# Optimization experiments

Measured on AMD Instinct MI355X. Metric: run time of the kernel, lower is better.

## Reference

```python
import jax, jax.numpy as jnp
import numpy as np

ISIZE = 512; NHEAD = 8; NNOD = 8; MAXP = 5; NEDGE = 34; TAU = 1.0; EPS = 1e-6
B = 4; SLEN = 1024

def _ln(x, g, b):
    m = x.mean(-1, keepdims=True)
    v = ((x - m) ** 2).mean(-1, keepdims=True)
    return (x - m) * jax.lax.rsqrt(v + EPS) * g + b

def _qmask(nsrc):
    # q_mask_full: edge 0 (encoder source) is masked out for the q path
    m = np.zeros((nsrc, 5), bool); m[0, :] = True
    return m.reshape(-1)

def _routing(node_p, edge_p):
    # Host-side argmax routing; mirrors the .item() syncs in the torch forward.
    node_p = np.asarray(node_p); edge_p = np.asarray(edge_p)
    routes, lind = [], 0
    for c in range(NNOD):
        nsrc = min(c + 2, MAXP); snode = c - nsrc
        ep = edge_p[:, lind:lind + nsrc, :].reshape(3, -1)
        qm = _qmask(nsrc)
        nact = int(np.argmax(node_p[c]))
        qsel = int(np.argmax(np.where(qm, -np.inf, ep[0])))
        r = dict(lind=lind, nsrc=nsrc, snode=snode, act=nact, q=qsel, k=None, v=None, ktype=None, km=None, vmode=None)
        if nact < 7:
            km = qm if nact > 0 else None
            kl = ep[1] if km is None else np.where(km, -np.inf, ep[1])
            r['k'] = int(np.argmax(kl)); r['km'] = km
            r['ktype'] = -2 if r['k'] // 5 == 0 else -1
            if nact < 5:
                if nact == 0 and r['ktype'] == -2:
                    r['v'] = int(np.argmax(ep[2][:5])); r['vmode'] = 'first5'
                else:
                    vl = ep[2] if km is None else np.where(km, -np.inf, ep[2])
                    r['v'] = int(np.argmax(vl)); r['vmode'] = 'full'
        routes.append(r); lind += nsrc
    return routes

def _selw(logits, mask, sel):
    # GumbleNormDrop (eval): softmax over masked logits, weight of selected entry
    if mask is not None:
        logits = jnp.where(jnp.asarray(mask), -jnp.inf, logits)
    return jax.nn.softmax(logits / TAU)[sel]

def _edge_op(x, e, op, eW, eb, eg, ebe):
    # ops 0/1/2: LN->Linear with relu/gelu/identity (cost isize^2+3*isize); 3: Linear; 4: identity
    if op == 4:
        return x
    if op == 3:
        return x @ eW[e] + eb[e]
    h = _ln(x, eg[e], ebe[e]) @ eW[e] + eb[e]
    return jax.nn.relu(h) if op == 0 else (jax.nn.gelu(h) if op == 1 else h)

def _mha(q, k, v, Wn, bn, gn, bln, mask):
    Bq, Sq, D = q.shape; dh = D // NHEAD; Sk = k.shape[1]
    qn = _ln(q, gn, bln)
    qh = (qn @ Wn[0] + bn[0]).reshape(Bq, Sq, NHEAD, dh).transpose(0, 2, 1, 3)
    kh = (k @ Wn[1] + bn[1]).reshape(Bq, Sk, NHEAD, dh).transpose(0, 2, 1, 3)
    vh = (v @ Wn[2] + bn[2]).reshape(Bq, v.shape[1], NHEAD, dh).transpose(0, 2, 1, 3)
    s = jnp.einsum('bhqd,bhkd->bhqk', qh, kh) / np.float32(np.sqrt(dh))
    if mask is not None:
        s = jnp.where(mask[:, :, None, :], -1e9, s)  # [B,1,Sk] -> [B,1,1,Sk]
    o = jnp.einsum('bhqk,bhkd->bhqd', jax.nn.softmax(s, -1), vh)
    o = o.transpose(0, 2, 1, 3).reshape(Bq, Sq, D)
    return q + o @ Wn[3] + bn[3]

def _node_op(q, k, v, act, Wn, bn, gn, bln, mask):
    if act == 0: return _mha(q, k, v, Wn, bn, gn, bln, mask)
    if act == 1: return q + (jax.nn.gelu(q @ Wn[0] + bn[0]) * (k @ Wn[1] + bn[1])) @ Wn[3] + bn[3]
    if act == 2: return _ln(q + k + v, gn, bln)
    if act == 3: return q + jax.nn.relu(q @ Wn[0] + k @ Wn[1] + v @ Wn[2]) @ Wn[3] + bn[3]
    if act == 4: return q * jax.nn.sigmoid(k) + v
    if act == 5: return q + jax.nn.gelu(k @ Wn[1] + bn[1])
    if act == 6: return q + k
    return _ln(q, gn, bln)  # act 7: unary

def _forward(inpute, inputo, node_p, edge_p, eW, eb, eg, ebe, nW, nb, ng, nbe, og, obe, src_pad_mask, tgt_pad_mask, routes):
    outs = {-2: inpute, -1: inputo}
    processed = set()
    for c, r in enumerate(routes):
        lind, snode = r['lind'], r['snode']
        epq, epk, epv = (edge_p[i, lind:lind + r['nsrc'], :].reshape(-1) for i in range(3))
        qm = _qmask(r['nsrc'])
        aw = jax.nn.softmax(node_p[c] / TAU)[r['act']]
        def take(sel, logits, mask):
            se, op = sel // 5, sel % 5
            inn = -2 if se == 0 else snode + se
            processed.add(inn)
            return _selw(logits, mask, sel) * _edge_op(outs[inn], lind + se, op, eW, eb, eg, ebe)
        qv = take(r['q'], epq, qm)
        kv = take(r['k'], epk, r['km']) if r['k'] is not None else None
        if r['v'] is None:
            vv = None
        elif r['vmode'] == 'first5':
            vv = take(r['v'], epv[:5], None)
        else:
            vv = take(r['v'], epv, r['km'])
        mask = None if r['act'] == 7 else (tgt_pad_mask if r['ktype'] == -1 else src_pad_mask)
        outs[c] = aw * _node_op(qv, kv, vv, r['act'], nW[c], nb[c], ng[c], nbe[c], mask)
    rem = [outs[i] for i in range(NNOD) if i not in processed]
    o = rem[0]
    for t in rem[1:]:
        o = o + t
    return _ln(o, og, obe)

def setup_inputs():
    key = jax.random.key(0)
    ks = jax.random.split(key, 8)
    s = 0.02
    return {
        'inpute': jax.random.normal(ks[0], (B, SLEN, ISIZE), jnp.float32),
        'inputo': jax.random.normal(ks[1], (B, SLEN, ISIZE), jnp.float32),
        'node_p': jax.random.normal(ks[2], (NNOD, 8), jnp.float32),
        'edge_p': jax.random.normal(ks[3], (3, NEDGE, 5), jnp.float32),
        'edge_W': jax.random.normal(ks[4], (NEDGE, ISIZE, ISIZE), jnp.float32) * s,
        'edge_b': jnp.zeros((NEDGE, ISIZE), jnp.float32),
        'edge_g': jnp.ones((NEDGE, ISIZE), jnp.float32),
        'edge_beta': jnp.zeros((NEDGE, ISIZE), jnp.float32),
        'node_W': jax.random.normal(ks[5], (NNOD, 4, ISIZE, ISIZE), jnp.float32) * s,
        'node_b': jnp.zeros((NNOD, 4, ISIZE), jnp.float32),
        'node_g': jnp.ones((NNOD, ISIZE), jnp.float32),
        'node_beta': jnp.zeros((NNOD, ISIZE), jnp.float32),
        'out_g': jnp.ones((ISIZE,), jnp.float32),
        'out_beta': jnp.zeros((ISIZE,), jnp.float32),
        'src_pad_mask': jnp.zeros((B, 1, SLEN), bool),
        'tgt_pad_mask': jnp.zeros((B, 1, SLEN), bool),
    }

def reference(inpute, inputo, node_p, edge_p, edge_W, edge_b, edge_g, edge_beta, node_W, node_b, node_g, node_beta, out_g, out_beta, src_pad_mask, tgt_pad_mask):
    routes = _routing(node_p, edge_p)
    return _forward(inpute, inputo, node_p, edge_p, edge_W, edge_b, edge_g, edge_beta, node_W, node_b, node_g, node_beta, out_g, out_beta, src_pad_mask, tgt_pad_mask, routes)
```

## Files before the change

### kernel.cpp

```cpp
#include <hip/hip_runtime.h>
#include <hip/hip_bf16.h>
#include <math.h>

#define NTOK 4096
#define DIM  512
#define NNODC 8
#define NEDGEC 34
#define NMAT  98
#define NBUF 4

typedef unsigned short u16;
typedef unsigned int   u32;

typedef __attribute__((ext_vector_type(8))) short bf16x8;
typedef __attribute__((ext_vector_type(4))) float f32x4;

__device__ __forceinline__ float b2f(u16 u){ return __uint_as_float(((u32)u) << 16); }
__device__ __forceinline__ u16 f2b(float f){
    u32 x = __float_as_uint(f);
    u32 r = x + 0x7FFFu + ((x >> 16) & 1u);
    return (u16)(r >> 16);
}
__device__ __forceinline__ float ldp(const void* p, int i, int isbf){
    return isbf ? b2f(((const u16*)p)[i]) : ((const float*)p)[i];
// ... 227 lines not shown
    const size_t base = ((size_t)blockIdx.x*256 + threadIdx.x) * 8;
    if (R->isbf){
        *(uint4*)(Xb0 + base) = *(const uint4*)((const u16*)ie + base);
        *(uint4*)(Xb1 + base) = *(const uint4*)((const u16*)io + base);
    } else {
        const float* a = (const float*)ie + base;
        const float* b = (const float*)io + base;
        u16 oa[8], ob[8];
        #pragma unroll
        for (int j = 0; j < 8; j++){ oa[j] = f2b(a[j]); ob[j] = f2b(b[j]); }
        *(uint4*)(Xb0 + base) = *(const uint4*)oa;
        *(uint4*)(Xb1 + base) = *(const uint4*)ob;
    }
}

struct __align__(16) LGS { u16 A[NBUF][64*64]; u16 B[NBUF][64*64]; };
struct __align__(16) LGU {
    union { LGS g; float st[64*68]; } u;
    float2 rowst[64];
};

__device__ void lean_gemm(LGU& smu, int isbf, int nsrc, int m0, int n0,
        const u16* __restrict__ A0, const u16* __restrict__ A1, const u16* __restrict__ A2,
        const u16* __restrict__ W0, const u16* __restrict__ W1, const u16* __restrict__ W2,
        const void* bias, int actMode,
        const float* __restrict__ uv,
        const u16* __restrict__ residB, float scale,
        u16* __restrict__ outB)
{
    LGS& sm = smu.u.g;
    const int tid = threadIdx.x;
    const int w = tid >> 6, lane = tid & 63;
    const int wr = w >> 1, wc = w & 1;
    const int l15 = lane & 15, quad = lane >> 4;
    const int NT = nsrc * 8;

    const int rsw = lane >> 3;
    const int c16 = lane & 7;
    const int rA  = w*16 + rsw;
    const int kx  = (c16 ^ rsw) << 3;

    auto stage = [&](int buf, int it){
        const int s = it >> 3, kt = it & 7;
        const u16* Ab = (s == 0) ? A0 : ((s == 1) ? A1 : A2);
        const u16* Wb = (s == 0) ? W0 : ((s == 1) ? W1 : W2);
        const size_t ka = (size_t)kt*64 + kx;
        const u16* ga = Ab + (size_t)(m0 + rA)*DIM + ka;
        const u16* gb = Wb + (size_t)(n0 + rA)*DIM + ka;
        u16* la = &sm.A[buf][rA*64 + c16*8];
        u16* lb = &sm.B[buf][rA*64 + c16*8];
        gload16(ga,          la);
        gload16(ga + 8*DIM,  la + 8*64);
        gload16(gb,          lb);
        gload16(gb + 8*DIM,  lb + 8*64);
    };

    f32x4 acc[2][2];
    #pragma unroll
    for (int i = 0; i < 2; i++)
        #pragma unroll
        for (int j = 0; j < 2; j++) acc[i][j] = (f32x4){0.f,0.f,0.f,0.f};

    float ssum = 0.f, ssq = 0.f;

    stage(0, 0);
    if (NT > 1) stage(1, 1);

    for (int it = 0; it < NT; it++){
        const int buf = it & (NBUF-1);
        if (it + 2 < NT) stage((it + 2) & (NBUF-1), it + 2);
        const int newer = (NT - 1 - it) < 2 ? (NT - 1 - it) : 2;
        if (newer == 2)      asm volatile("s_waitcnt vmcnt(8)" ::: "memory");
        else if (newer == 1) asm volatile("s_waitcnt vmcnt(4)" ::: "memory");
        else                 asm volatile("s_waitcnt vmcnt(0)" ::: "memory");
        __builtin_amdgcn_s_barrier();
        __builtin_amdgcn_sched_barrier(0);
        #pragma unroll
        for (int kc = 0; kc < 2; kc++){
            const int sl = (((kc*4 + quad) ^ (l15 & 7)) << 3);
            bf16x8 af0 = *(const bf16x8*)&sm.A[buf][(wr*32      + l15)*64 + sl];
            bf16x8 af1 = *(const bf16x8*)&sm.A[buf][(wr*32 + 16 + l15)*64 + sl];
            bf16x8 bf0 = *(const bf16x8*)&sm.B[buf][(wc*32      + l15)*64 + sl];
            bf16x8 bf1 = *(const bf16x8*)&sm.B[buf][(wc*32 + 16 + l15)*64 + sl];
            acc[0][0] = __builtin_amdgcn_mfma_f32_16x16x32_bf16(af0, bf0, acc[0][0], 0, 0, 0);
            acc[0][1] = __builtin_amdgcn_mfma_f32_16x16x32_bf16(af0, bf1, acc[0][1], 0, 0, 0);
            acc[1][0] = __builtin_amdgcn_mfma_f32_16x16x32_bf16(af1, bf0, acc[1][0], 0, 0, 0);
            acc[1][1] = __builtin_amdgcn_mfma_f32_16x16x32_bf16(af1, bf1, acc[1][1], 0, 0, 0);
        }
        if (uv){
            const int srow = w*16 + l15;
            #pragma unroll
            for (int ch = 0; ch < 2; ch++){
                const int gc = quad*2 + ch;
                const bf16x8 xv = *(const bf16x8*)&sm.A[buf][srow*64 + ((gc ^ (srow&7))<<3)];
                #pragma unroll
                for (int t2 = 0; t2 < 8; t2++){
                    const float fx = b2f((u16)xv[t2]);
                    ssum += fx; ssq += fx*fx;
                }
            }
        }
    }

    if (uv){
        ssum += __shfl_xor(ssum, 16); ssq += __shfl_xor(ssq, 16);
        ssum += __shfl_xor(ssum, 32); ssq += __shfl_xor(ssq, 32);
        if (quad == 0){
            const float mu = ssum*(1.0f/512.0f);
            const float rstd = rsqrtf(ssq*(1.0f/512.0f) - mu*mu + 1e-6f);
            smu.rowst[w*16 + l15] = make_float2(mu, rstd);
        }
    }
    __syncthreads();

    float* st = smu.u.st;
    #pragma unroll
    for (int i = 0; i < 2; i++){
        const int rowl = wr*32 + i*16 + quad*4;
        float al[4], bet[4];
        if (uv){
            #pragma unroll
            for (int rg = 0; rg < 4; rg++){
                const float2 ms = smu.rowst[rowl + rg];
                al[rg] = ms.y; bet[rg] = -ms.y*ms.x;
            }
        }
        #pragma unroll
        for (int j = 0; j < 2; j++){
            const int coll = wc*32 + j*16 + l15;
            const float bv = bias ? ldp(bias, n0 + coll, isbf) : 0.f;
            const float un = uv ? uv[n0 + coll]       : 0.f;
            const float vn = uv ? uv[512 + n0 + coll] : 0.f;
            #pragma unroll
            for (int rg = 0; rg < 4; rg++){
                float v = acc[i][j][rg];
                if (uv) v = al[rg]*v + bet[rg]*un + vn;
                v += bv;
                if (actMode == 1) v = fmaxf(v, 0.f);
                else if (actMode == 2) v = gelu_t(v);
                st[(rowl + rg)*68 + coll] = v;
            }
        }
    }
    __syncthreads();
    #pragma unroll
    for (int t = 0; t < 2; t++){
        const int cid = tid + 256*t;
        const int rowl = cid >> 3, cg = (cid & 7)*8;
        float v[8];
        *(float4*)&v[0] = *(const float4*)&st[rowl*68 + cg];
        *(float4*)&v[4] = *(const float4*)&st[rowl*68 + cg + 4];
        const size_t go = (size_t)(m0 + rowl)*DIM + n0 + cg;
        if (residB){
            uint4 ru = *(const uint4*)(residB + go);
            const u16* rp = (const u16*)&ru;
            #pragma unroll
            for (int j2 = 0; j2 < 8; j2++) v[j2] += b2f(rp[j2]);
        }
        u16 o[8];
        #pragma unroll
        for (int j2 = 0; j2 < 8; j2++) o[j2] = f2b(v[j2]*scale);
        *(uint4*)(outB + go) = *(const uint4*)o;
    }
}

__device__ __forceinline__ void tile_remap(int* m0, int* n0){
    const int lin = blockIdx.y*64 + blockIdx.x;
    const int xcd = lin & 7, idx = lin >> 3;
    *m0 = (xcd*8 + (idx & 7)) * 64;
    *n0 = (idx >> 3) * 64;
}

__device__ __forceinline__ const void* subp(const void* p, size_t elemOff, int isbf){
    return isbf ? (const void*)((const u16*)p + elemOff) : (const void*)((const float*)p + elemOff);
}

__global__ __launch_bounds__(256, 2) void edge_gemm(const Routes* __restrict__ R, int c,
        const u16* __restrict__ Xb,
        u16* QVb, u16* KVb, u16* VVb,
        const u16* __restrict__ Wt, const float* __restrict__ UV, const void* eb){
    __shared__ LGU sm;
    const int isbf = R->isbf;
    const int z = blockIdx.z;
    int has, slot, e, op; float w; u16* outB;
    if (z == 0){ has = 1;            slot = R->q_slot[c]; e = R->q_e[c]; op = R->q_op[c]; w = R->qw[c]; outB = QVb; }
    else if (z == 1){ has = R->k_has[c]; slot = R->k_slot[c]; e = R->k_e[c]; op = R->k_op[c]; w = R->kw[c]; outB = KVb; }
    else        { has = R->v_has[c]; slot = R->v_slot[c]; e = R->v_e[c]; op = R->v_op[c]; w = R->vw[c]; outB = VVb; }
    if (!has) return;
    if (op == 4){
        const int tid = threadIdx.x;
        const int r  = blockIdx.x*64 + (tid >> 2);
        const int c0 = blockIdx.y*64 + (tid & 3)*16;
        const u16* src = Xb + (size_t)slot*NTOK*DIM + (size_t)r*DIM + c0;
        const size_t off = (size_t)r*DIM + c0;
        #pragma unroll
        for (int t = 0; t < 2; t++){
            uint4 u = *(const uint4*)(src + t*8);
            const u16* up = (const u16*)&u;
            u16 o[8];
            #pragma unroll
            for (int j = 0; j < 8; j++) o[j] = f2b(w*b2f(up[j]));
            *(uint4*)(outB + off + t*8) = *(const uint4*)o;
        }
        return;
    }
    const u16* A = Xb + (size_t)slot*NTOK*DIM;
    int m0, n0; tile_remap(&m0, &n0);
    const size_t msz = (size_t)DIM*DIM;
    if (op < 3){
        const int f = c*3 + z;
        const int actMode = (op == 0) ? 1 : ((op == 1) ? 2 : 0);
        lean_gemm(sm, isbf, 1, m0, n0, A, nullptr, nullptr,
                  Wt + (size_t)(66 + f)*msz, nullptr, nullptr,
                  subp(eb, (size_t)e*DIM, isbf), actMode,
                  UV + (size_t)f*1024, nullptr, w, outB);
    } else {
        lean_gemm(sm, isbf, 1, m0, n0, A, nullptr, nullptr,
                  Wt + (size_t)e*msz, nullptr, nullptr,
                  subp(eb, (size_t)e*DIM, isbf), 0,
                  nullptr, nullptr, w, outB);
    }
}

__global__ __launch_bounds__(256) void mid1(const Routes* __restrict__ R, int c,
        const u16* __restrict__ QVb, const u16* __restrict__ KVb, const u16* __restrict__ VVb,
        u16* __restrict__ outcb,
        const void* ng, const void* nbeta){
    const int act = R->act[c];
    if (act == 0 || act == 1 || act == 3 || act == 5) return;
    const int isbf = R->isbf;
    const float aw = R->aw[c];
    const int tid = threadIdx.x, wid = tid >> 6, lane = tid & 63;
    const int row = blockIdx.x*4 + wid;
    const size_t roff = (size_t)row*DIM;
    float x[8];
    #pragma unroll
    for (int j = 0; j < 2; j++){
        ushort4 u = *(const ushort4*)(QVb + roff + lane*4 + j*256);
        x[j*4+0] = b2f(u.x); x[j*4+1] = b2f(u.y); x[j*4+2] = b2f(u.z); x[j*4+3] = b2f(u.w);
    }
    if (act == 4 || act == 6 || act == 2){
        float k[8], v[8];
        #pragma unroll
        for (int j = 0; j < 2; j++){
            ushort4 u = *(const ushort4*)(KVb + roff + lane*4 + j*256);
            k[j*4+0] = b2f(u.x); k[j*4+1] = b2f(u.y); k[j*4+2] = b2f(u.z); k[j*4+3] = b2f(u.w);
        }
        if (act != 6){
            #pragma unroll
            for (int j = 0; j < 2; j++){
                ushort4 u = *(const ushort4*)(VVb + roff + lane*4 + j*256);
                v[j*4+0] = b2f(u.x); v[j*4+1] = b2f(u.y); v[j*4+2] = b2f(u.z); v[j*4+3] = b2f(u.w);
            }
        }
        if (act == 4){
            #pragma unroll
            for (int j = 0; j < 2; j++){
                u16 o[4];
                #pragma unroll
                for (int t = 0; t < 4; t++) o[t] = f2b(aw*(x[j*4+t]*sigm(k[j*4+t]) + v[j*4+t]));
                *(ushort4*)(outcb + roff + lane*4 + j*256) = *(const ushort4*)o;
            }
            return;
        }
        if (act == 6){
            #pragma unroll
            for (int j = 0; j < 2; j++){
                u16 o[4];
                #pragma unroll
                for (int t = 0; t < 4; t++) o[t] = f2b(aw*(x[j*4+t] + k[j*4+t]));
                *(ushort4*)(outcb + roff + lane*4 + j*256) = *(const ushort4*)o;
            }
            return;
        }
        #pragma unroll
        for (int j = 0; j < 8; j++) x[j] += k[j] + v[j];
    }
    float s = 0.f, q2 = 0.f;
    #pragma unroll
    for (int j = 0; j < 8; j++){ s += x[j]; q2 += x[j]*x[j]; }
    #pragma unroll
    for (int m = 1; m < 64; m <<= 1){ s += __shfl_xor(s, m); q2 += __shfl_xor(q2, m); }
    const float mu = s*(1.0f/512.0f);
    const float rstd = rsqrtf(q2*(1.0f/512.0f) - mu*mu + 1e-6f);
    #pragma unroll
    for (int j = 0; j < 2; j++){
        const int col = lane*4 + j*256;
        u16 o[4];
        #pragma unroll
        for (int t = 0; t < 4; t++)
            o[t] = f2b(aw*((x[j*4+t] - mu)*rstd*ldp(ng, c*DIM + col + t, isbf) + ldp(nbeta, c*DIM + col + t, isbf)));
        *(ushort4*)(outcb + roff + col) = *(const ushort4*)o;
    }
}

__global__ __launch_bounds__(256, 2) void node_gemm_a(const Routes* __restrict__ R, int c,
        const u16* __restrict__ QVb, const u16* __restrict__ KVb, const u16* __restrict__ VVb,
        u16* T1b, u16* T2b, u16* T3b,
        const u16* __restrict__ Wt, const float* __restrict__ UV, const void* nb){
    __shared__ LGU sm;
    const int isbf = R->isbf;
    const int act = R->act[c];
    const int z = blockIdx.z;
    const size_t msz = (size_t)DIM*DIM;
    const u16* W0 = Wt + (NEDGEC + (size_t)c*4 + 0)*msz;
    const u16* W1 = Wt + (NEDGEC + (size_t)c*4 + 1)*msz;
    const u16* W2 = Wt + (NEDGEC + (size_t)c*4 + 2)*msz;
// ... 18 lines not shown
            lean_gemm(sm, isbf, 1, m0, n0, KVb,0,0, W1,0,0, b1, 2, nullptr, nullptr, 1.f, T2b);
    } else {
        if (act == 0)
            lean_gemm(sm, isbf, 1, m0, n0, VVb,0,0, W2,0,0, b2, 0, nullptr, nullptr, 1.f, T3b);
    }
}

struct __align__(16) FS {
    float Qs[64][68];
    float KPs[64][68];
    float Vs[64][68];
    float red[64*16];
    float mrun[64], lrun[64], alph[64];
};

__global__ __launch_bounds__(256) void mid2(const Routes* __restrict__ R, int c,
        const u16* __restrict__ Q, const u16* __restrict__ K,
        const u16* __restrict__ V, u16* __restrict__ T4b){
    const int act = R->act[c];
    if (act == 1){
        const int bid = blockIdx.y*32 + blockIdx.x;
        const size_t base = ((size_t)bid*256 + threadIdx.x)*16;
        #pragma unroll
        for (int h = 0; h < 2; h++){
            uint4 ua = *(const uint4*)(Q + base + h*8);
            uint4 ub = *(const uint4*)(K + base + h*8);
            const u16* pa = (const u16*)&ua;
            const u16* pb = (const u16*)&ub;
            u16 o[8];
            #pragma unroll
            for (int j = 0; j < 8; j++) o[j] = f2b(b2f(pa[j]) * b2f(pb[j]));
            *(uint4*)(T4b + base + h*8) = *(const uint4*)o;
        }
        return;
    }
    if (act != 0) return;
    __shared__ FS sm;
    const int tid = threadIdx.x;
    const int tx = tid & 15, ty = tid >> 4;
    const int b = blockIdx.x >> 3, h = blockIdx.x & 7;
    const int q0 = blockIdx.y * 64;
    const size_t baseQ = ((size_t)b*1024 + q0)*DIM + h*64;
    {
        const int r = tid >> 2, ch = tid & 3;
        const u16* qp = Q + baseQ + (size_t)r*DIM + ch*16;
        #pragma unroll
        for (int t = 0; t < 4; t++){
            ushort4 u = *(const ushort4*)(qp + t*4);
            sm.Qs[r][ch*16 + t*4 + 0] = b2f(u.x);
            sm.Qs[r][ch*16 + t*4 + 1] = b2f(u.y);
            sm.Qs[r][ch*16 + t*4 + 2] = b2f(u.z);
            sm.Qs[r][ch*16 + t*4 + 3] = b2f(u.w);
        }
    }
    if (tid < 64){ sm.mrun[tid] = -INFINITY; sm.lrun[tid] = 0.f; }
    float o[4][4];
    #pragma unroll
    for (int i = 0; i < 4; i++)
        #pragma unroll
        for (int j = 0; j < 4; j++) o[i][j] = 0.f;
    __syncthreads();

    for (int kt = 0; kt < 16; kt++){
        const size_t baseK = ((size_t)b*1024 + kt*64)*DIM + h*64;
        {
            const int r = tid >> 2, ch = tid & 3;
            const u16* kp = K + baseK + (size_t)r*DIM + ch*16;
            const u16* vp = V + baseK + (size_t)r*DIM + ch*16;
            #pragma unroll
            for (int t = 0; t < 4; t++){
                ushort4 uk = *(const ushort4*)(kp + t*4);
                ushort4 uv2 = *(const ushort4*)(vp + t*4);
                sm.KPs[r][ch*16 + t*4 + 0] = b2f(uk.x);
                sm.KPs[r][ch*16 + t*4 + 1] = b2f(uk.y);
                sm.KPs[r][ch*16 + t*4 + 2] = b2f(uk.z);
                sm.KPs[r][ch*16 + t*4 + 3] = b2f(uk.w);
                sm.Vs [r][ch*16 + t*4 + 0] = b2f(uv2.x);
                sm.Vs [r][ch*16 + t*4 + 1] = b2f(uv2.y);
                sm.Vs [r][ch*16 + t*4 + 2] = b2f(uv2.z);
                sm.Vs [r][ch*16 + t*4 + 3] = b2f(uv2.w);
            }
        }
        __syncthreads();
        float s[4][4];
        #pragma unroll
        for (int i = 0; i < 4; i++)
            #pragma unroll
            for (int j = 0; j < 4; j++) s[i][j] = 0.f;
        for (int d = 0; d < 64; d += 4){
            float4 qv[4], kv[4];
            #pragma unroll
            for (int i = 0; i < 4; i++) qv[i] = *(const float4*)&sm.Qs[ty*4+i][d];
            #pragma unroll
            for (int j = 0; j < 4; j++) kv[j] = *(const float4*)&sm.KPs[tx*4+j][d];
            #pragma unroll
            for (int i = 0; i < 4; i++)
                #pragma unroll
                for (int j = 0; j < 4; j++)
                    s[i][j] += qv[i].x*kv[j].x + qv[i].y*kv[j].y + qv[i].z*kv[j].z + qv[i].w*kv[j].w;
        }
        #pragma unroll
        for (int i = 0; i < 4; i++)
            #pragma unroll
            for (int j = 0; j < 4; j++) s[i][j] *= 0.125f;
        #pragma unroll
        for (int i = 0; i < 4; i++){
            float mx = fmaxf(fmaxf(s[i][0], s[i][1]), fmaxf(s[i][2], s[i][3]));
            sm.red[(ty*4+i)*16 + tx] = mx;
        }
        __syncthreads();
        if (tid < 64){
            float mt = -INFINITY;
            for (int t = 0; t < 16; t++) mt = fmaxf(mt, sm.red[tid*16+t]);
            float mold = sm.mrun[tid];
            float mnew = fmaxf(mold, mt);
            sm.alph[tid] = expf(mold - mnew);
            sm.mrun[tid] = mnew;
        }
        __syncthreads();
        #pragma unroll
        for (int i = 0; i < 4; i++){
            const float mn = sm.mrun[ty*4+i];
            float ps = 0.f;
            #pragma unroll
            for (int j = 0; j < 4; j++){
                float p = expf(s[i][j] - mn);
                sm.KPs[ty*4+i][tx*4+j] = p;
                ps += p;
            }
            sm.red[(ty*4+i)*16 + tx] = ps;
        }
        __syncthreads();
        if (tid < 64){
            float ss = 0.f;
            for (int t = 0; t < 16; t++) ss += sm.red[tid*16+t];
            sm.lrun[tid] = sm.lrun[tid]*sm.alph[tid] + ss;
        }
        __syncthreads();
        #pragma unroll
        for (int i = 0; i < 4; i++){
            const float a = sm.alph[ty*4+i];
            #pragma unroll
            for (int j = 0; j < 4; j++) o[i][j] *= a;
        }
        for (int k = 0; k < 64; k++){
            float4 v4 = *(const float4*)&sm.Vs[k][tx*4];
            float p0 = sm.KPs[ty*4+0][k];
            float p1 = sm.KPs[ty*4+1][k];
            float p2 = sm.KPs[ty*4+2][k];
            float p3 = sm.KPs[ty*4+3][k];
            o[0][0] += p0*v4.x; o[0][1] += p0*v4.y; o[0][2] += p0*v4.z; o[0][3] += p0*v4.w;
            o[1][0] += p1*v4.x; o[1][1] += p1*v4.y; o[1][2] += p1*v4.z; o[1][3] += p1*v4.w;
            o[2][0] += p2*v4.x; o[2][1] += p2*v4.y; o[2][2] += p2*v4.z; o[2][3] += p2*v4.w;
            o[3][0] += p3*v4.x; o[3][1] += p3*v4.y; o[3][2] += p3*v4.z; o[3][3] += p3*v4.w;
        }
        __syncthreads();
    }
    #pragma unroll
    for (int i = 0; i < 4; i++){
        const float inv = 1.0f / sm.lrun[ty*4+i];
        u16 ov[4];
        #pragma unroll
        for (int j = 0; j < 4; j++) ov[j] = f2b(o[i][j]*inv);
        *(ushort4*)(T4b + baseQ + (size_t)(ty*4+i)*DIM + tx*4) = *(const ushort4*)ov;
    }
}

__global__ __launch_bounds__(256, 2) void node_gemm_b(const Routes* __restrict__ R, int c,
        const u16* __restrict__ QVb, const u16* __restrict__ T1b,
        const u16* __restrict__ T4b, const u16* __restrict__ T2b,
        u16* outcb, const u16* __restrict__ Wt, const void* nb){
    const int act = R->act[c];
    const float aw = R->aw[c];
    if (act == 5){
        const int tid = threadIdx.x;
        const int r  = blockIdx.x*64 + (tid >> 2);
        const int c0 = blockIdx.y*64 + (tid & 3)*16;
        const size_t off = (size_t)r*DIM + c0;
        #pragma unroll
        for (int t = 0; t < 2; t++){
            uint4 uq = *(const uint4*)(QVb + off + t*8);
            uint4 ug = *(const uint4*)(T2b + off + t*8);
            const u16* pq = (const u16*)&uq;
            const u16* pg = (const u16*)&ug;
            u16 o[8];
            #pragma unroll
            for (int j = 0; j < 8; j++) o[j] = f2b(aw*(b2f(pq[j]) + b2f(pg[j])));
            *(uint4*)(outcb + off + t*8) = *(const uint4*)o;
        }
        return;
    }
    if (!(act == 0 || act == 1 || act == 3)) return;
    __shared__ LGU sm;
    const int isbf = R->isbf;
    const u16* W3 = Wt + (NEDGEC + (size_t)c*4 + 3)*(size_t)DIM*DIM;
    const void* b3 = subp(nb, (size_t)(c*4 + 3)*DIM, isbf);
    const u16* A = (act == 3) ? T1b : T4b;
    int m0, n0; tile_remap(&m0, &n0);
    lean_gemm(sm, isbf, 1, m0, n0, A, nullptr, nullptr, W3, nullptr, nullptr,
              b3, 0, nullptr, QVb, aw, outcb);
}

__global__ __launch_bounds__(128) void final_ln(const Routes* __restrict__ R,
        const u16* __restrict__ Xb, const void* og, const void* obeta,
        void* __restrict__ out){
    const int isbf = R->isbf;
    const int row = blockIdx.x, tid = threadIdx.x;
    const size_t off = (size_t)row*DIM + tid*4;
    float x0 = 0.f, x1 = 0.f, x2 = 0.f, x3 = 0.f;
// ... 57 lines not shown
    u16* KVb = (u16*)p; p += SZ*2;
    u16* VVb = (u16*)p; p += SZ*2;
    u16* T1b = (u16*)p; p += SZ*2;
    u16* T2b = (u16*)p; p += SZ*2;
    u16* T3b = (u16*)p; p += SZ*2;
    u16* T4b = (u16*)p; p += SZ*2;

    routing_kernel<<<1, 64, 0, stream>>>(node_p, edge_p, (const u32*)eg, R);
    transpose_w<<<dim3(16, 16, NMAT), 256, 0, stream>>>(R, eW, nW, eg, ng, (const u32*)eg, Wt);
    calc_uv_part<<<dim3(32, 8), 512, 0, stream>>>(R, eW, nW, eg, ebeta, ng, nbeta, UVp);
    reduce_uv<<<32, 512, 0, stream>>>(R, UVp, UV);
    convert_in<<<1024, 256, 0, stream>>>(R, inpute, inputo, Xb, Xb + SZ);

    for (int c = 0; c < NNODC; c++){
        u16* outcb = Xb + (size_t)(2 + c)*SZ;
        edge_gemm  <<<dim3(64, 8, 3), 256, 0, stream>>>(R, c, Xb, QVb, KVb, VVb, Wt, UV, eb);
        mid1       <<<1024, 256, 0, stream>>>(R, c, QVb, KVb, VVb, outcb, ng, nbeta);
        node_gemm_a<<<dim3(64, 8, 3), 256, 0, stream>>>(R, c, QVb, KVb, VVb, T1b, T2b, T3b, Wt, UV, nb);
        mid2       <<<dim3(32, 16), 256, 0, stream>>>(R, c, T1b, T2b, T3b, T4b);
        node_gemm_b<<<dim3(64, 8), 256, 0, stream>>>(R, c, QVb, T1b, T4b, T2b, outcb, Wt, nb);
    }
    final_ln<<<4096, 128, 0, stream>>>(R, Xb, og, obeta, d_out);
}
```

Baseline: 487.4 us.

## Enlarge GEMM tiles to 128x128 and merge mid kernels into one launch

The shared GEMM routine moves from 64x64 tiles with a 4-deep prefetch ring to 128x128 tiles with double buffering, giving each wave a 4x4 block of MFMA accumulators and more operand reuse per LDS load. The tile remap, grids and LN statistics gathering are updated to match. The two elementwise/attention mid kernels are merged into one launch, and the act==5 path moves out of node_gemm_b into it, cutting launches per node. The cost is fewer blocks per GEMM (128 instead of 512 per z-slice), a shallower prefetch pipeline, and higher register and LDS use that may lower occupancy.

```diff
diff --git a/kernel.cpp b/kernel.cpp
--- a/kernel.cpp
+++ b/kernel.cpp
@@ -7,7 +7,6 @@
 #define NNODC 8
 #define NEDGEC 34
 #define NMAT  98
-#define NBUF 4
 
 typedef unsigned short u16;
 typedef unsigned int   u32;
@@ -265,10 +264,10 @@
     }
 }
 
-struct __align__(16) LGS { u16 A[NBUF][64*64]; u16 B[NBUF][64*64]; };
+struct __align__(16) LGS { u16 A[2][128*64]; u16 B[2][128*64]; };
 struct __align__(16) LGU {
-    union { LGS g; float st[64*68]; } u;
-    float2 rowst[64];
+    union { LGS g; float st[128*132]; } u;
+    float2 rowst[128];
 };
 
 __device__ void lean_gemm(LGU& smu, int isbf, int nsrc, int m0, int n0,
@@ -288,7 +287,7 @@
 
     const int rsw = lane >> 3;
     const int c16 = lane & 7;
-    const int rA  = w*16 + rsw;
+    const int rA  = w*8 + rsw;
     const int kx  = (c16 ^ rsw) << 3;
 
     auto stage = [&](int buf, int it){
@@ -296,54 +295,52 @@
         const u16* Ab = (s == 0) ? A0 : ((s == 1) ? A1 : A2);
         const u16* Wb = (s == 0) ? W0 : ((s == 1) ? W1 : W2);
         const size_t ka = (size_t)kt*64 + kx;
-        const u16* ga = Ab + (size_t)(m0 + rA)*DIM + ka;
-        const u16* gb = Wb + (size_t)(n0 + rA)*DIM + ka;
-        u16* la = &sm.A[buf][rA*64 + c16*8];
-        u16* lb = &sm.B[buf][rA*64 + c16*8];
-        gload16(ga,          la);
-        gload16(ga + 8*DIM,  la + 8*64);
-        gload16(gb,          lb);
-        gload16(gb + 8*DIM,  lb + 8*64);
+        #pragma unroll
+        for (int i = 0; i < 4; i++){
+            const int r = rA + i*32;
+            gload16(Ab + (size_t)(m0 + r)*DIM + ka, &sm.A[buf][r*64 + c16*8]);
+            gload16(Wb + (size_t)(n0 + r)*DIM + ka, &sm.B[buf][r*64 + c16*8]);
+        }
     };
 
-    f32x4 acc[2][2];
-    #pragma unroll
-    for (int i = 0; i < 2; i++)
-        #pragma unroll
-        for (int j = 0; j < 2; j++) acc[i][j] = (f32x4){0.f,0.f,0.f,0.f};
+    f32x4 acc[4][4];
+    #pragma unroll
+    for (int i = 0; i < 4; i++)
+        #pragma unroll
+        for (int j = 0; j < 4; j++) acc[i][j] = (f32x4){0.f,0.f,0.f,0.f};
 
     float ssum = 0.f, ssq = 0.f;
+    const int frow = tid >> 1, fhalf = tid & 1;
 
     stage(0, 0);
-    if (NT > 1) stage(1, 1);
 
     for (int it = 0; it < NT; it++){
-        const int buf = it & (NBUF-1);
-        if (it + 2 < NT) stage((it + 2) & (NBUF-1), it + 2);
-        const int newer = (NT - 1 - it) < 2 ? (NT - 1 - it) : 2;
-        if (newer == 2)      asm volatile("s_waitcnt vmcnt(8)" ::: "memory");
-        else if (newer == 1) asm volatile("s_waitcnt vmcnt(4)" ::: "memory");
-        else                 asm volatile("s_waitcnt vmcnt(0)" ::: "memory");
+        const int buf = it & 1;
+        asm volatile("s_waitcnt vmcnt(0)" ::: "memory");
         __builtin_amdgcn_s_barrier();
         __builtin_amdgcn_sched_barrier(0);
+        if (it + 1 < NT) stage(buf ^ 1, it + 1);
         #pragma unroll
         for (int kc = 0; kc < 2; kc++){
-            const int sl = (((kc*4 + quad) ^ (l15 & 7)) << 3);
-            bf16x8 af0 = *(const bf16x8*)&sm.A[buf][(wr*32      + l15)*64 + sl];
-            bf16x8 af1 = *(const bf16x8*)&sm.A[buf][(wr*32 + 16 + l15)*64 + sl];
-            bf16x8 bf0 = *(const bf16x8*)&sm.B[buf][(wc*32      + l15)*64 + sl];
-            bf16x8 bf1 = *(const bf16x8*)&sm.B[buf][(wc*32 + 16 + l15)*64 + sl];
-            acc[0][0] = __builtin_amdgcn_mfma_f32_16x16x32_bf16(af0, bf0, acc[0][0], 0, 0, 0);
-            acc[0][1] = __builtin_amdgcn_mfma_f32_16x16x32_bf16(af0, bf1, acc[0][1], 0, 0, 0);
-            acc[1][0] = __builtin_amdgcn_mfma_f32_16x16x32_bf16(af1, bf0, acc[1][0], 0, 0, 0);
-            acc[1][1] = __builtin_amdgcn_mfma_f32_16x16x32_bf16(af1, bf1, acc[1][1], 0, 0, 0);
+            const int sl = ((kc*4 + quad) ^ (l15 & 7)) << 3;
+            bf16x8 af[4], bv[4];
+            #pragma unroll
+            for (int i = 0; i < 4; i++)
+                af[i] = *(const bf16x8*)&sm.A[buf][(wr*64 + i*16 + l15)*64 + sl];
+            #pragma unroll
+            for (int j = 0; j < 4; j++)
+                bv[j] = *(const bf16x8*)&sm.B[buf][(wc*64 + j*16 + l15)*64 + sl];
+            #pragma unroll
+            for (int i = 0; i < 4; i++)
+                #pragma unroll
+                for (int j = 0; j < 4; j++)
+                    acc[i][j] = __builtin_amdgcn_mfma_f32_16x16x32_bf16(af[i], bv[j], acc[i][j], 0, 0, 0);
         }
         if (uv){
-            const int srow = w*16 + l15;
-            #pragma unroll
-            for (int ch = 0; ch < 2; ch++){
-                const int gc = quad*2 + ch;
-                const bf16x8 xv = *(const bf16x8*)&sm.A[buf][srow*64 + ((gc ^ (srow&7))<<3)];
+            #pragma unroll
+            for (int ch = 0; ch < 4; ch++){
+                const int gc = fhalf*4 + ch;
+                const bf16x8 xv = *(const bf16x8*)&sm.A[buf][frow*64 + ((gc ^ (frow&7))<<3)];
                 #pragma unroll
                 for (int t2 = 0; t2 < 8; t2++){
                     const float fx = b2f((u16)xv[t2]);
@@ -354,20 +351,19 @@
     }
 
     if (uv){
-        ssum += __shfl_xor(ssum, 16); ssq += __shfl_xor(ssq, 16);
-        ssum += __shfl_xor(ssum, 32); ssq += __shfl_xor(ssq, 32);
-        if (quad == 0){
+        ssum += __shfl_xor(ssum, 1); ssq += __shfl_xor(ssq, 1);
+        if (fhalf == 0){
             const float mu = ssum*(1.0f/512.0f);
             const float rstd = rsqrtf(ssq*(1.0f/512.0f) - mu*mu + 1e-6f);
-            smu.rowst[w*16 + l15] = make_float2(mu, rstd);
+            smu.rowst[frow] = make_float2(mu, rstd);
         }
     }
     __syncthreads();
 
     float* st = smu.u.st;
     #pragma unroll
-    for (int i = 0; i < 2; i++){
-        const int rowl = wr*32 + i*16 + quad*4;
+    for (int i = 0; i < 4; i++){
+        const int rowl = wr*64 + i*16 + quad*4;
         float al[4], bet[4];
         if (uv){
             #pragma unroll
@@ -377,8 +373,8 @@
             }
         }
         #pragma unroll
-        for (int j = 0; j < 2; j++){
-            const int coll = wc*32 + j*16 + l15;
+        for (int j = 0; j < 4; j++){
+            const int coll = wc*64 + j*16 + l15;
             const float bv = bias ? ldp(bias, n0 + coll, isbf) : 0.f;
             const float un = uv ? uv[n0 + coll]       : 0.f;
             const float vn = uv ? uv[512 + n0 + coll] : 0.f;
@@ -389,18 +385,18 @@
                 v += bv;
                 if (actMode == 1) v = fmaxf(v, 0.f);
                 else if (actMode == 2) v = gelu_t(v);
-                st[(rowl + rg)*68 + coll] = v;
+                st[(rowl + rg)*132 + coll] = v;
             }
         }
     }
     __syncthreads();
     #pragma unroll
-    for (int t = 0; t < 2; t++){
+    for (int t = 0; t < 8; t++){
         const int cid = tid + 256*t;
-        const int rowl = cid >> 3, cg = (cid & 7)*8;
+        const int rowl = cid >> 4, cg = (cid & 15)*8;
         float v[8];
-        *(float4*)&v[0] = *(const float4*)&st[rowl*68 + cg];
-        *(float4*)&v[4] = *(const float4*)&st[rowl*68 + cg + 4];
+        *(float4*)&v[0] = *(const float4*)&st[rowl*132 + cg];
+        *(float4*)&v[4] = *(const float4*)&st[rowl*132 + cg + 4];
         const size_t go = (size_t)(m0 + rowl)*DIM + n0 + cg;
         if (residB){
             uint4 ru = *(const uint4*)(residB + go);
@@ -416,10 +412,10 @@
 }
 
 __device__ __forceinline__ void tile_remap(int* m0, int* n0){
-    const int lin = blockIdx.y*64 + blockIdx.x;
+    const int lin = blockIdx.y*32 + blockIdx.x;
     const int xcd = lin & 7, idx = lin >> 3;
-    *m0 = (xcd*8 + (idx & 7)) * 64;
-    *n0 = (idx >> 3) * 64;
+    *m0 = (xcd*4 + (idx & 3)) * 128;
+    *n0 = (idx >> 2) * 128;
 }
 
 __device__ __forceinline__ const void* subp(const void* p, size_t elemOff, int isbf){
@@ -440,18 +436,18 @@
     if (!has) return;
     if (op == 4){
         const int tid = threadIdx.x;
-        const int r  = blockIdx.x*64 + (tid >> 2);
-        const int c0 = blockIdx.y*64 + (tid & 3)*16;
+        const int r  = blockIdx.x*128 + (tid >> 1);
+        const int c0 = blockIdx.y*128 + (tid & 1)*64;
         const u16* src = Xb + (size_t)slot*NTOK*DIM + (size_t)r*DIM + c0;
-        const size_t off = (size_t)r*DIM + c0;
-        #pragma unroll
-        for (int t = 0; t < 2; t++){
+        u16* dst = outB + (size_t)r*DIM + c0;
+        #pragma unroll
+        for (int t = 0; t < 8; t++){
             uint4 u = *(const uint4*)(src + t*8);
             const u16* up = (const u16*)&u;
             u16 o[8];
             #pragma unroll
             for (int j = 0; j < 8; j++) o[j] = f2b(w*b2f(up[j]));
-            *(uint4*)(outB + off + t*8) = *(const uint4*)o;
+            *(uint4*)(dst + t*8) = *(const uint4*)o;
         }
         return;
     }
@@ -470,78 +466,6 @@
                   Wt + (size_t)e*msz, nullptr, nullptr,
                   subp(eb, (size_t)e*DIM, isbf), 0,
                   nullptr, nullptr, w, outB);
-    }
-}
-
-__global__ __launch_bounds__(256) void mid1(const Routes* __restrict__ R, int c,
-        const u16* __restrict__ QVb, const u16* __restrict__ KVb, const u16* __restrict__ VVb,
-        u16* __restrict__ outcb,
-        const void* ng, const void* nbeta){
-    const int act = R->act[c];
-    if (act == 0 || act == 1 || act == 3 || act == 5) return;
-    const int isbf = R->isbf;
-    const float aw = R->aw[c];
-    const int tid = threadIdx.x, wid = tid >> 6, lane = tid & 63;
-    const int row = blockIdx.x*4 + wid;
-    const size_t roff = (size_t)row*DIM;
-    float x[8];
-    #pragma unroll
-    for (int j = 0; j < 2; j++){
-        ushort4 u = *(const ushort4*)(QVb + roff + lane*4 + j*256);
-        x[j*4+0] = b2f(u.x); x[j*4+1] = b2f(u.y); x[j*4+2] = b2f(u.z); x[j*4+3] = b2f(u.w);
-    }
-    if (act == 4 || act == 6 || act == 2){
-        float k[8], v[8];
-        #pragma unroll
-        for (int j = 0; j < 2; j++){
-            ushort4 u = *(const ushort4*)(KVb + roff + lane*4 + j*256);
-            k[j*4+0] = b2f(u.x); k[j*4+1] = b2f(u.y); k[j*4+2] = b2f(u.z); k[j*4+3] = b2f(u.w);
-        }
-        if (act != 6){
-            #pragma unroll
-            for (int j = 0; j < 2; j++){
-                ushort4 u = *(const ushort4*)(VVb + roff + lane*4 + j*256);
-                v[j*4+0] = b2f(u.x); v[j*4+1] = b2f(u.y); v[j*4+2] = b2f(u.z); v[j*4+3] = b2f(u.w);
-            }
-        }
-        if (act == 4){
-            #pragma unroll
-            for (int j = 0; j < 2; j++){
-                u16 o[4];
-                #pragma unroll
-                for (int t = 0; t < 4; t++) o[t] = f2b(aw*(x[j*4+t]*sigm(k[j*4+t]) + v[j*4+t]));
-                *(ushort4*)(outcb + roff + lane*4 + j*256) = *(const ushort4*)o;
-            }
-            return;
-        }
-        if (act == 6){
-            #pragma unroll
-            for (int j = 0; j < 2; j++){
-                u16 o[4];
-                #pragma unroll
-                for (int t = 0; t < 4; t++) o[t] = f2b(aw*(x[j*4+t] + k[j*4+t]));
-                *(ushort4*)(outcb + roff + lane*4 + j*256) = *(const ushort4*)o;
-            }
-            return;
-        }
-        #pragma unroll
-        for (int j = 0; j < 8; j++) x[j] += k[j] + v[j];
-    }
-    float s = 0.f, q2 = 0.f;
-    #pragma unroll
-    for (int j = 0; j < 8; j++){ s += x[j]; q2 += x[j]*x[j]; }
-    #pragma unroll
-    for (int m = 1; m < 64; m <<= 1){ s += __shfl_xor(s, m); q2 += __shfl_xor(q2, m); }
-    const float mu = s*(1.0f/512.0f);
-    const float rstd = rsqrtf(q2*(1.0f/512.0f) - mu*mu + 1e-6f);
-    #pragma unroll
-    for (int j = 0; j < 2; j++){
-        const int col = lane*4 + j*256;
-        u16 o[4];
-        #pragma unroll
-        for (int t = 0; t < 4; t++)
-            o[t] = f2b(aw*((x[j*4+t] - mu)*rstd*ldp(ng, c*DIM + col + t, isbf) + ldp(nbeta, c*DIM + col + t, isbf)));
-        *(ushort4*)(outcb + roff + col) = *(const ushort4*)o;
     }
 }
 
@@ -590,185 +514,244 @@
     float mrun[64], lrun[64], alph[64];
 };
 
-__global__ __launch_bounds__(256) void mid2(const Routes* __restrict__ R, int c,
-        const u16* __restrict__ Q, const u16* __restrict__ K,
-        const u16* __restrict__ V, u16* __restrict__ T4b){
+__global__ __launch_bounds__(256) void mid(const Routes* __restrict__ R, int c,
+        const u16* __restrict__ QVb, const u16* __restrict__ KVb, const u16* __restrict__ VVb,
+        const u16* __restrict__ T1b, const u16* __restrict__ T2b, const u16* __restrict__ T3b,
+        u16* __restrict__ T4b, u16* __restrict__ outcb,
+        const void* ng, const void* nbeta){
+    __shared__ FS sm;
     const int act = R->act[c];
-    if (act == 1){
-        const int bid = blockIdx.y*32 + blockIdx.x;
-        const size_t base = ((size_t)bid*256 + threadIdx.x)*16;
-        #pragma unroll
-        for (int h = 0; h < 2; h++){
-            uint4 ua = *(const uint4*)(Q + base + h*8);
-            uint4 ub = *(const uint4*)(K + base + h*8);
-            const u16* pa = (const u16*)&ua;
-            const u16* pb = (const u16*)&ub;
-            u16 o[8];
+    if (act == 3) return;
+    const int tid = threadIdx.x;
+    const float aw = R->aw[c];
+
+    if (act == 1 || act == 5){
+        const int bid = blockIdx.y*64 + blockIdx.x;
+        const size_t base = ((size_t)bid*256 + tid)*8;
+        uint4 ua = *(const uint4*)(((act == 1) ? T1b : QVb) + base);
+        uint4 ub = *(const uint4*)(T2b + base);
+        const u16* pa = (const u16*)&ua;
+        const u16* pb = (const u16*)&ub;
+        u16 o[8];
+        if (act == 1){
             #pragma unroll
             for (int j = 0; j < 8; j++) o[j] = f2b(b2f(pa[j]) * b2f(pb[j]));
-            *(uint4*)(T4b + base + h*8) = *(const uint4*)o;
+            *(uint4*)(T4b + base) = *(const uint4*)o;
+        } else {
+            #pragma unroll
+            for (int j = 0; j < 8; j++) o[j] = f2b(aw*(b2f(pa[j]) + b2f(pb[j])));
+            *(uint4*)(outcb + base) = *(const uint4*)o;
         }
         return;
     }
-    if (act != 0) return;
-    __shared__ FS sm;
-    const int tid = threadIdx.x;
-    const int tx = tid & 15, ty = tid >> 4;
-    const int b = blockIdx.x >> 3, h = blockIdx.x & 7;
-    const int q0 = blockIdx.y * 64;
-    const size_t baseQ = ((size_t)b*1024 + q0)*DIM + h*64;
-    {
-        const int r = tid >> 2, ch = tid & 3;
-        const u16* qp = Q + baseQ + (size_t)r*DIM + ch*16;
-        #pragma unroll
-        for (int t = 0; t < 4; t++){
-            ushort4 u = *(const ushort4*)(qp + t*4);
-            sm.Qs[r][ch*16 + t*4 + 0] = b2f(u.x);
-            sm.Qs[r][ch*16 + t*4 + 1] = b2f(u.y);
-            sm.Qs[r][ch*16 + t*4 + 2] = b2f(u.z);
-            sm.Qs[r][ch*16 + t*4 + 3] = b2f(u.w);
-        }
-    }
-    if (tid < 64){ sm.mrun[tid] = -INFINITY; sm.lrun[tid] = 0.f; }
-    float o[4][4];
-    #pragma unroll
-    for (int i = 0; i < 4; i++)
-        #pragma unroll
-        for (int j = 0; j < 4; j++) o[i][j] = 0.f;
-    __syncthreads();
-
-    for (int kt = 0; kt < 16; kt++){
-        const size_t baseK = ((size_t)b*1024 + kt*64)*DIM + h*64;
+
+    if (act == 0){
+        if (blockIdx.x >= 32) return;
+        const int tx = tid & 15, ty = tid >> 4;
+        const int b = blockIdx.x >> 3, h = blockIdx.x & 7;
+        const int q0 = blockIdx.y * 64;
+        const size_t baseQ = ((size_t)b*1024 + q0)*DIM + h*64;
         {
             const int r = tid >> 2, ch = tid & 3;
-            const u16* kp = K + baseK + (size_t)r*DIM + ch*16;
-            const u16* vp = V + baseK + (size_t)r*DIM + ch*16;
+            const u16* qp = T1b + baseQ + (size_t)r*DIM + ch*16;
             #pragma unroll
             for (int t = 0; t < 4; t++){
-                ushort4 uk = *(const ushort4*)(kp + t*4);
-                ushort4 uv2 = *(const ushort4*)(vp + t*4);
-                sm.KPs[r][ch*16 + t*4 + 0] = b2f(uk.x);
-                sm.KPs[r][ch*16 + t*4 + 1] = b2f(uk.y);
-                sm.KPs[r][ch*16 + t*4 + 2] = b2f(uk.z);
-                sm.KPs[r][ch*16 + t*4 + 3] = b2f(uk.w);
-                sm.Vs [r][ch*16 + t*4 + 0] = b2f(uv2.x);
-                sm.Vs [r][ch*16 + t*4 + 1] = b2f(uv2.y);
-                sm.Vs [r][ch*16 + t*4 + 2] = b2f(uv2.z);
-                sm.Vs [r][ch*16 + t*4 + 3] = b2f(uv2.w);
-            }
-        }
+                ushort4 u = *(const ushort4*)(qp + t*4);
+                sm.Qs[r][ch*16 + t*4 + 0] = b2f(u.x);
+                sm.Qs[r][ch*16 + t*4 + 1] = b2f(u.y);
+                sm.Qs[r][ch*16 + t*4 + 2] = b2f(u.z);
+                sm.Qs[r][ch*16 + t*4 + 3] = b2f(u.w);
+            }
+        }
+        if (tid < 64){ sm.mrun[tid] = -INFINITY; sm.lrun[tid] = 0.f; }
+        float o[4][4];
+        #pragma unroll
+        for (int i = 0; i < 4; i++)
+            #pragma unroll
+            for (int j = 0; j < 4; j++) o[i][j] = 0.f;
         __syncthreads();
-        float s[4][4];
-        #pragma unroll
-        for (int i = 0; i < 4; i++)
-            #pragma unroll
-            for (int j = 0; j < 4; j++) s[i][j] = 0.f;
-        for (int d = 0; d < 64; d += 4){
-            float4 qv[4], kv[4];
-            #pragma unroll
-            for (int i = 0; i < 4; i++) qv[i] = *(const float4*)&sm.Qs[ty*4+i][d];
-            #pragma unroll
-            for (int j = 0; j < 4; j++) kv[j] = *(const float4*)&sm.KPs[tx*4+j][d];
+
+        for (int kt = 0; kt < 16; kt++){
+            const size_t baseK = ((size_t)b*1024 + kt*64)*DIM + h*64;
+            {
+                const int r = tid >> 2, ch = tid & 3;
+                const u16* kp = T2b + baseK + (size_t)r*DIM + ch*16;
+                const u16* vp = T3b + baseK + (size_t)r*DIM + ch*16;
+                #pragma unroll
+                for (int t = 0; t < 4; t++){
+                    ushort4 uk = *(const ushort4*)(kp + t*4);
+                    ushort4 uv2 = *(const ushort4*)(vp + t*4);
+                    sm.KPs[r][ch*16 + t*4 + 0] = b2f(uk.x);
+                    sm.KPs[r][ch*16 + t*4 + 1] = b2f(uk.y);
+                    sm.KPs[r][ch*16 + t*4 + 2] = b2f(uk.z);
+                    sm.KPs[r][ch*16 + t*4 + 3] = b2f(uk.w);
+                    sm.Vs [r][ch*16 + t*4 + 0] = b2f(uv2.x);
+                    sm.Vs [r][ch*16 + t*4 + 1] = b2f(uv2.y);
+                    sm.Vs [r][ch*16 + t*4 + 2] = b2f(uv2.z);
+                    sm.Vs [r][ch*16 + t*4 + 3] = b2f(uv2.w);
+                }
+            }
+            __syncthreads();
+            float s[4][4];
             #pragma unroll
             for (int i = 0; i < 4; i++)
                 #pragma unroll
-                for (int j = 0; j < 4; j++)
-                    s[i][j] += qv[i].x*kv[j].x + qv[i].y*kv[j].y + qv[i].z*kv[j].z + qv[i].w*kv[j].w;
-        }
-        #pragma unroll
-        for (int i = 0; i < 4; i++)
-            #pragma unroll
-            for (int j = 0; j < 4; j++) s[i][j] *= 0.125f;
+                for (int j = 0; j < 4; j++) s[i][j] = 0.f;
+            for (int d = 0; d < 64; d += 4){
+                float4 qv[4], kv[4];
+                #pragma unroll
+                for (int i = 0; i < 4; i++) qv[i] = *(const float4*)&sm.Qs[ty*4+i][d];
+                #pragma unroll
+                for (int j = 0; j < 4; j++) kv[j] = *(const float4*)&sm.KPs[tx*4+j][d];
+                #pragma unroll
+                for (int i = 0; i < 4; i++)
+                    #pragma unroll
+                    for (int j = 0; j < 4; j++)
+                        s[i][j] += qv[i].x*kv[j].x + qv[i].y*kv[j].y + qv[i].z*kv[j].z + qv[i].w*kv[j].w;
+            }
+            #pragma unroll
+            for (int i = 0; i < 4; i++)
+                #pragma unroll
+                for (int j = 0; j < 4; j++) s[i][j] *= 0.125f;
+            #pragma unroll
+            for (int i = 0; i < 4; i++){
+                float mx = fmaxf(fmaxf(s[i][0], s[i][1]), fmaxf(s[i][2], s[i][3]));
+                sm.red[(ty*4+i)*16 + tx] = mx;
+            }
+            __syncthreads();
+            if (tid < 64){
+                float mt = -INFINITY;
+                for (int t = 0; t < 16; t++) mt = fmaxf(mt, sm.red[tid*16+t]);
+                float mold = sm.mrun[tid];
+                float mnew = fmaxf(mold, mt);
+                sm.alph[tid] = expf(mold - mnew);
+                sm.mrun[tid] = mnew;
+            }
+            __syncthreads();
+            #pragma unroll
+            for (int i = 0; i < 4; i++){
+                const float mn = sm.mrun[ty*4+i];
+                float ps = 0.f;
+                #pragma unroll
+                for (int j = 0; j < 4; j++){
+                    float p = expf(s[i][j] - mn);
+                    sm.KPs[ty*4+i][tx*4+j] = p;
+                    ps += p;
+                }
+                sm.red[(ty*4+i)*16 + tx] = ps;
+            }
+            __syncthreads();
+            if (tid < 64){
+                float ss = 0.f;
+                for (int t = 0; t < 16; t++) ss += sm.red[tid*16+t];
+                sm.lrun[tid] = sm.lrun[tid]*sm.alph[tid] + ss;
+            }
+            __syncthreads();
+            #pragma unroll
+            for (int i = 0; i < 4; i++){
+                const float a = sm.alph[ty*4+i];
+                #pragma unroll
+                for (int j = 0; j < 4; j++) o[i][j] *= a;
+            }
+            for (int k = 0; k < 64; k++){
+                float4 v4 = *(const float4*)&sm.Vs[k][tx*4];
+                float p0 = sm.KPs[ty*4+0][k];
+                float p1 = sm.KPs[ty*4+1][k];
+                float p2 = sm.KPs[ty*4+2][k];
+                float p3 = sm.KPs[ty*4+3][k];
+                o[0][0] += p0*v4.x; o[0][1] += p0*v4.y; o[0][2] += p0*v4.z; o[0][3] += p0*v4.w;
+                o[1][0] += p1*v4.x; o[1][1] += p1*v4.y; o[1][2] += p1*v4.z; o[1][3] += p1*v4.w;
+                o[2][0] += p2*v4.x; o[2][1] += p2*v4.y; o[2][2] += p2*v4.z; o[2][3] += p2*v4.w;
+                o[3][0] += p3*v4.x; o[3][1] += p3*v4.y; o[3][2] += p3*v4.z; o[3][3] += p3*v4.w;
+            }
+            __syncthreads();
+        }
         #pragma unroll
         for (int i = 0; i < 4; i++){
-            float mx = fmaxf(fmaxf(s[i][0], s[i][1]), fmaxf(s[i][2], s[i][3]));
-            sm.red[(ty*4+i)*16 + tx] = mx;
-        }
-        __syncthreads();
-        if (tid < 64){
-            float mt = -INFINITY;
-            for (int t = 0; t < 16; t++) mt = fmaxf(mt, sm.red[tid*16+t]);
-            float mold = sm.mrun[tid];
-            float mnew = fmaxf(mold, mt);
-            sm.alph[tid] = expf(mold - mnew);
-            sm.mrun[tid] = mnew;
-        }
-        __syncthreads();
-        #pragma unroll
-        for (int i = 0; i < 4; i++){
-            const float mn = sm.mrun[ty*4+i];
-            float ps = 0.f;
-            #pragma unroll
-            for (int j = 0; j < 4; j++){
-                float p = expf(s[i][j] - mn);
-                sm.KPs[ty*4+i][tx*4+j] = p;
-                ps += p;
-            }
-            sm.red[(ty*4+i)*16 + tx] = ps;
-        }
-        __syncthreads();
-        if (tid < 64){
-            float ss = 0.f;
-            for (int t = 0; t < 16; t++) ss += sm.red[tid*16+t];
-            sm.lrun[tid] = sm.lrun[tid]*sm.alph[tid] + ss;
-        }
-        __syncthreads();
-        #pragma unroll
-        for (int i = 0; i < 4; i++){
-            const float a = sm.alph[ty*4+i];
-            #pragma unroll
-            for (int j = 0; j < 4; j++) o[i][j] *= a;
-        }
-        for (int k = 0; k < 64; k++){
-            float4 v4 = *(const float4*)&sm.Vs[k][tx*4];
-            float p0 = sm.KPs[ty*4+0][k];
-            float p1 = sm.KPs[ty*4+1][k];
-            float p2 = sm.KPs[ty*4+2][k];
-            float p3 = sm.KPs[ty*4+3][k];
-            o[0][0] += p0*v4.x; o[0][1] += p0*v4.y; o[0][2] += p0*v4.z; o[0][3] += p0*v4.w;
-            o[1][0] += p1*v4.x; o[1][1] += p1*v4.y; o[1][2] += p1*v4.z; o[1][3] += p1*v4.w;
-            o[2][0] += p2*v4.x; o[2][1] += p2*v4.y; o[2][2] += p2*v4.z; o[2][3] += p2*v4.w;
-            o[3][0] += p3*v4.x; o[3][1] += p3*v4.y; o[3][2] += p3*v4.z; o[3][3] += p3*v4.w;
-        }
-        __syncthreads();
-    }
-    #pragma unroll
-    for (int i = 0; i < 4; i++){
-        const float inv = 1.0f / sm.lrun[ty*4+i];
-        u16 ov[4];
-        #pragma unroll
-        for (int j = 0; j < 4; j++) ov[j] = f2b(o[i][j]*inv);
-        *(ushort4*)(T4b + baseQ + (size_t)(ty*4+i)*DIM + tx*4) = *(const ushort4*)ov;
+            const float inv = 1.0f / sm.lrun[ty*4+i];
+            u16 ov[4];
+            #pragma unroll
+            for (int j = 0; j < 4; j++) ov[j] = f2b(o[i][j]*inv);
+            *(ushort4*)(T4b + baseQ + (size_t)(ty*4+i)*DIM + tx*4) = *(const ushort4*)ov;
+        }
+        return;
+    }
+
+    const int isbf = R->isbf;
+    const int wid = tid >> 6, lane = tid & 63;
+    const int bid = blockIdx.y*64 + blockIdx.x;
+    const int row = bid*4 + wid;
+    const size_t roff = (size_t)row*DIM;
+    float x[8];
+    #pragma unroll
+    for (int j = 0; j < 2; j++){
+        ushort4 u = *(const ushort4*)(QVb + roff + lane*4 + j*256);
+        x[j*4+0] = b2f(u.x); x[j*4+1] = b2f(u.y); x[j*4+2] = b2f(u.z); x[j*4+3] = b2f(u.w);
+    }
+    if (act == 4 || act == 6 || act == 2){
+        float k[8], v[8];
+        #pragma unroll
+        for (int j = 0; j < 2; j++){
+            ushort4 u = *(const ushort4*)(KVb + roff + lane*4 + j*256);
+            k[j*4+0] = b2f(u.x); k[j*4+1] = b2f(u.y); k[j*4+2] = b2f(u.z); k[j*4+3] = b2f(u.w);
+        }
+        if (act != 6){
+            #pragma unroll
+            for (int j = 0; j < 2; j++){
+                ushort4 u = *(const ushort4*)(VVb + roff + lane*4 + j*256);
+                v[j*4+0] = b2f(u.x); v[j*4+1] = b2f(u.y); v[j*4+2] = b2f(u.z); v[j*4+3] = b2f(u.w);
+            }
+        }
+        if (act == 4){
+            #pragma unroll
+            for (int j = 0; j < 2; j++){
+                u16 o[4];
+                #pragma unroll
+                for (int t = 0; t < 4; t++) o[t] = f2b(aw*(x[j*4+t]*sigm(k[j*4+t]) + v[j*4+t]));
+                *(ushort4*)(outcb + roff + lane*4 + j*256) = *(const ushort4*)o;
+            }
+            return;
+        }
+        if (act == 6){
+            #pragma unroll
+            for (int j = 0; j < 2; j++){
+                u16 o[4];
+                #pragma unroll
+                for (int t = 0; t < 4; t++) o[t] = f2b(aw*(x[j*4+t] + k[j*4+t]));
+                *(ushort4*)(outcb + roff + lane*4 + j*256) = *(const ushort4*)o;
+            }
+            return;
+        }
+        #pragma unroll
+        for (int j = 0; j < 8; j++) x[j] += k[j] + v[j];
+    }
+    float s = 0.f, q2 = 0.f;
+    #pragma unroll
+    for (int j = 0; j < 8; j++){ s += x[j]; q2 += x[j]*x[j]; }
+    #pragma unroll
+    for (int m = 1; m < 64; m <<= 1){ s += __shfl_xor(s, m); q2 += __shfl_xor(q2, m); }
+    const float mu = s*(1.0f/512.0f);
+    const float rstd = rsqrtf(q2*(1.0f/512.0f) - mu*mu + 1e-6f);
+    #pragma unroll
+    for (int j = 0; j < 2; j++){
+        const int col = lane*4 + j*256;
+        u16 o[4];
+        #pragma unroll
+        for (int t = 0; t < 4; t++)
+            o[t] = f2b(aw*((x[j*4+t] - mu)*rstd*ldp(ng, c*DIM + col + t, isbf) + ldp(nbeta, c*DIM + col + t, isbf)));
+        *(ushort4*)(outcb + roff + col) = *(const ushort4*)o;
     }
 }
 
 __global__ __launch_bounds__(256, 2) void node_gemm_b(const Routes* __restrict__ R, int c,
         const u16* __restrict__ QVb, const u16* __restrict__ T1b,
-        const u16* __restrict__ T4b, const u16* __restrict__ T2b,
+        const u16* __restrict__ T4b,
         u16* outcb, const u16* __restrict__ Wt, const void* nb){
     const int act = R->act[c];
-    const float aw = R->aw[c];
-    if (act == 5){
-        const int tid = threadIdx.x;
-        const int r  = blockIdx.x*64 + (tid >> 2);
-        const int c0 = blockIdx.y*64 + (tid & 3)*16;
-        const size_t off = (size_t)r*DIM + c0;
-        #pragma unroll
-        for (int t = 0; t < 2; t++){
-            uint4 uq = *(const uint4*)(QVb + off + t*8);
-            uint4 ug = *(const uint4*)(T2b + off + t*8);
-            const u16* pq = (const u16*)&uq;
-            const u16* pg = (const u16*)&ug;
-            u16 o[8];
-            #pragma unroll
-            for (int j = 0; j < 8; j++) o[j] = f2b(aw*(b2f(pq[j]) + b2f(pg[j])));
-            *(uint4*)(outcb + off + t*8) = *(const uint4*)o;
-        }
-        return;
-    }
     if (!(act == 0 || act == 1 || act == 3)) return;
     __shared__ LGU sm;
     const int isbf = R->isbf;
+    const float aw = R->aw[c];
     const u16* W3 = Wt + (NEDGEC + (size_t)c*4 + 3)*(size_t)DIM*DIM;
     const void* b3 = subp(nb, (size_t)(c*4 + 3)*DIM, isbf);
     const u16* A = (act == 3) ? T1b : T4b;
@@ -856,11 +839,10 @@
 
     for (int c = 0; c < NNODC; c++){
         u16* outcb = Xb + (size_t)(2 + c)*SZ;
-        edge_gemm  <<<dim3(64, 8, 3), 256, 0, stream>>>(R, c, Xb, QVb, KVb, VVb, Wt, UV, eb);
-        mid1       <<<1024, 256, 0, stream>>>(R, c, QVb, KVb, VVb, outcb, ng, nbeta);
-        node_gemm_a<<<dim3(64, 8, 3), 256, 0, stream>>>(R, c, QVb, KVb, VVb, T1b, T2b, T3b, Wt, UV, nb);
-        mid2       <<<dim3(32, 16), 256, 0, stream>>>(R, c, T1b, T2b, T3b, T4b);
-        node_gemm_b<<<dim3(64, 8), 256, 0, stream>>>(R, c, QVb, T1b, T4b, T2b, outcb, Wt, nb);
+        edge_gemm  <<<dim3(32, 4, 3), 256, 0, stream>>>(R, c, Xb, QVb, KVb, VVb, Wt, UV, eb);
+        node_gemm_a<<<dim3(32, 4, 3), 256, 0, stream>>>(R, c, QVb, KVb, VVb, T1b, T2b, T3b, Wt, UV, nb);
+        mid        <<<dim3(64, 16), 256, 0, stream>>>(R, c, QVb, KVb, VVb, T1b, T2b, T3b, T4b, outcb, ng, nbeta);
+        node_gemm_b<<<dim3(32, 4), 256, 0, stream>>>(R, c, QVb, T1b, T4b, outcb, Wt, nb);
     }
     final_ln<<<4096, 128, 0, stream>>>(R, Xb, og, obeta, d_out);
 }
```

Result: slower. 657.9 us (+35.0%).
